# Kernel tuning notes

Hardware: AMD Instinct MI355X
Metric: run time of the kernel (lower is better)

Reference implementation:

```python
import jax, jax.numpy as jnp
import numpy as np

FILTER_WIDTH = 23
NSIG = 9.0
RATIO = 4.0
SUB_LOW_RATIO = 1.0
PCT = 3.0  # normalization_percentile_threshold


def _gaussian_kernel_2d(ksize, sigma):
    # matches cv2.getGaussianKernel for sigma > 0: normalized 1D gaussian, outer product
    i = np.arange(ksize, dtype=np.float64) - (ksize - 1) / 2.0
    k1 = np.exp(-(i ** 2) / (2.0 * sigma ** 2))
    k1 /= k1.sum()
    k2 = np.outer(k1, k1)
    return k2.astype(np.float32)


def setup_inputs() -> dict:
    key = jax.random.key(0)
    k1, k2 = jax.random.split(key)
    x = jax.random.normal(k1, (16, 3, 512, 512), dtype=jnp.float32)
    mask = jax.random.uniform(k2, (16, 1, 512, 512), dtype=jnp.float32)
    kernel = jnp.asarray(_gaussian_kernel_2d(FILTER_WIDTH, NSIG))[None, None]  # [1,1,23,23]
    return {"x": x, "mask": mask, "kernel": kernel}


def reference(x, mask, kernel):
    N, C, H, W = x.shape
    pad = FILTER_WIDTH // 2  # 11

    # --- median padding (torch.median = lower median -> sorted index (n-1)//2) ---
    flat = x.reshape(N, C, H * W)
    med = jnp.sort(flat, axis=-1)[:, :, (H * W - 1) // 2] + 0.2  # [N,C]
    med = med[:, :, None, None]
    xp = mask * x + (1.0 - mask) * med  # [N,C,H,W]

    # --- Gaussian low-pass: replication pad + depthwise conv (same kernel per channel) ---
    xpad = jnp.pad(xp, ((0, 0), (0, 0), (pad, pad), (pad, pad)), mode="edge")
    k = jnp.broadcast_to(kernel, (C, 1, FILTER_WIDTH, FILTER_WIDTH))
    gauss = jax.lax.conv_general_dilated(
        xpad, k, window_strides=(1, 1), padding="VALID", feature_group_count=C
    )  # [N,C,H,W]

    res = RATIO * (xp - SUB_LOW_RATIO * gauss)

    # --- per-(n,c) percentile normalization on 1/256-quantized copy ---
    temp = jnp.trunc(res * 256.0) / 256.0  # torch .int() truncates toward zero
    tflat = temp.reshape(N, C, H * W)
    lo = jnp.percentile(tflat, PCT, axis=-1)[:, :, None, None]
    hi = jnp.percentile(tflat, 100.0 - PCT, axis=-1)[:, :, None, None]
    res = (res - lo) / (hi - lo)

    # sub_mask=True
    return res * mask
```

## Files before the change

### kernel.cpp

```cpp
#include <hip/hip_runtime.h>

#define HW 262144
#define WID 512
#define PLANES 48
#define NCH 3
#define PAD 11
#define FW 23
#define XS 92

__device__ __forceinline__ float uniform_f(float v) {
  return __uint_as_float((unsigned)__builtin_amdgcn_readfirstlane((int)__float_as_uint(v)));
}

__global__ __launch_bounds__(256) void hist1_kernel(const float* __restrict__ x,
                                                    int* __restrict__ ghist1) {
  __shared__ int h[8192];
  const int p = blockIdx.x, s = blockIdx.y, tid = threadIdx.x;
  for (int i = tid; i < 8192; i += 256) h[i] = 0;
  __syncthreads();
  const float4* xv = (const float4*)(x + (size_t)p * HW + (size_t)s * (HW / 16));
#define H1(c) { int b = (int)(((c) + 8.0f) * 512.0f); b = min(max(b, 0), 8191); atomicAdd(&h[b], 1); }
  for (int i = tid; i < HW / 16 / 4; i += 256) {
    float4 v = xv[i];
    H1(v.x); H1(v.y); H1(v.z); H1(v.w);
  }
#undef H1
  __syncthreads();
  int* gh = ghist1 + p * 8192;
  const int st = (s * 512) & 8191;
  for (int k = tid; k < 8192; k += 256) {
    int i = (k + st) & 8191;
    int c = h[i];
    if (c) atomicAdd(&gh[i], c);
  }
}

__global__ __launch_bounds__(256) void scan_med_kernel(const int* __restrict__ ghist1,
                                                       float* __restrict__ med,
                                                       const float* __restrict__ kern,
                                                       float* __restrict__ k1g) {
  __shared__ int incl[256];
  __shared__ int s_chunk, s_base;
  const int p = blockIdx.x, t = threadIdx.x;
  if (p == 0 && t < FW) k1g[t] = kern[t * FW + PAD] / sqrtf(kern[PAD * FW + PAD]);
  const int* gh = ghist1 + p * 8192;
  int mysum = 0;
#pragma unroll
  for (int j = 0; j < 32; ++j) mysum += gh[t * 32 + j];
  incl[t] = mysum;
  __syncthreads();
  for (int off = 1; off < 256; off <<= 1) {
    int v = (t >= off) ? incl[t - off] : 0;
    __syncthreads();
    incl[t] += v;
    __syncthreads();
  }
  const int rank = 131072;
  {
    int excl = incl[t] - mysum;
    if (excl < rank && rank <= incl[t]) { s_chunk = t; s_base = rank - excl; }
  }
  __syncthreads();
  if (t < 64) {
    const int c = s_chunk, base = s_base;
    int cnt = (t < 32) ? gh[c * 32 + t] : 0;
    int pfx = cnt;
#pragma unroll
    for (int off = 1; off < 32; off <<= 1) {
      int u = __shfl_up(pfx, off, 64);
      if (t >= off) pfx += u;
    }
    unsigned long long m = __ballot(t < 32 && pfx >= base);
    int bin = c * 32 + (__ffsll((long long)m) - 1);
    if (t == 0) med[p] = -8.0f + ((float)bin + 0.5f) * 0.001953125f + 0.2f;
  }
}

__global__ __launch_bounds__(256) void conv_kernel(const float* __restrict__ x,
                                                   const float* __restrict__ mask,
                                                   const float* __restrict__ k1g,
                                                   const float* __restrict__ med,
                                                   float* __restrict__ res) {
  __shared__ float xs[86 * XS];
  const int z = blockIdx.z;
  const int n = z / NCH;
  const int tbx = blockIdx.x, tby = blockIdx.y;
  const int tid = threadIdx.x;

  float k1[FW];
#pragma unroll
  for (int t = 0; t < FW; ++t) k1[t] = uniform_f(k1g[t]);

  const float m_med = uniform_f(med[z]);
  const int gr0 = tby * 64 - PAD;
  const int gc0 = tbx * 64 - PAD;
  const float* xb = x + (size_t)z * HW;
  const float* mb = mask + (size_t)n * HW;
  for (int i = tid; i < 86 * 86; i += 256) {
    int r = i / 86, c = i - r * 86;
    int gr = min(max(gr0 + r, 0), WID - 1);
    int gc = min(max(gc0 + c, 0), WID - 1);
    int g = gr * WID + gc;
    float xv = xb[g], mv = mb[g];
    xs[r * XS + c] = fmaf(mv, xv - m_med, m_med);
  }
  __syncthreads();

  float ah[3][8];
#pragma unroll
  for (int it = 0; it < 3; ++it) {
    const int g = tid + (it << 8);
    if (g < 86 * 8) {
      const int r = g >> 3, c0 = (g & 7) << 3;
      const float* row = &xs[r * XS + c0];
      float w[32];
#pragma unroll
      for (int q = 0; q < 8; ++q) *(float4*)&w[q * 4] = *(const float4*)(row + q * 4);
#pragma unroll
      for (int j = 0; j < 8; ++j) ah[it][j] = 0.f;
#pragma unroll
      for (int t = 0; t < FW; ++t) {
        const float k = k1[t];
#pragma unroll
        for (int j = 0; j < 8; ++j) ah[it][j] = fmaf(k, w[t + j], ah[it][j]);
      }
    }
  }

  const int ct = (tid & 15) << 2;
  const int rt = (tid >> 4) << 2;
  float4 xpA[4], xpB[4];
#pragma unroll
  for (int j = 0; j < 4; ++j) {
    const float* xr = &xs[(rt + j + PAD) * XS + ct];
    xpA[j] = *(const float4*)(xr + 8);
    xpB[j] = *(const float4*)(xr + 12);
  }
  __syncthreads();

#pragma unroll
  for (int it = 0; it < 3; ++it) {
    const int g = tid + (it << 8);
    if (g < 86 * 8) {
      const int r = g >> 3, c0 = (g & 7) << 3;
      *(float4*)&xs[r * XS + c0] = make_float4(ah[it][0], ah[it][1], ah[it][2], ah[it][3]);
      *(float4*)&xs[r * XS + c0 + 4] = make_float4(ah[it][4], ah[it][5], ah[it][6], ah[it][7]);
    }
  }
  __syncthreads();

  float4 acc[4];
#pragma unroll
  for (int j = 0; j < 4; ++j) acc[j] = make_float4(0.f, 0.f, 0.f, 0.f);
#pragma unroll
  for (int tp = 0; tp < 26; ++tp) {
    float4 v = *(const float4*)&xs[(rt + tp) * XS + ct];
    const int jlo = (tp - 22 > 0) ? (tp - 22) : 0;
    const int jhi = (tp < 3) ? tp : 3;
#pragma unroll
    for (int j = jlo; j <= jhi; ++j) {
      float k = k1[tp - j];
      acc[j].x = fmaf(k, v.x, acc[j].x);
      acc[j].y = fmaf(k, v.y, acc[j].y);
      acc[j].z = fmaf(k, v.z, acc[j].z);
      acc[j].w = fmaf(k, v.w, acc[j].w);
    }
  }

  float* rb = res + (size_t)z * HW + (size_t)(tby * 64 + rt) * WID + tbx * 64 + ct;
#pragma unroll
  for (int j = 0; j < 4; ++j) {
    float4 o;
    o.x = 4.0f * (xpA[j].w - acc[j].x);
    o.y = 4.0f * (xpB[j].x - acc[j].y);
    o.z = 4.0f * (xpB[j].y - acc[j].z);
    o.w = 4.0f * (xpB[j].z - acc[j].w);
    *(float4*)(rb + (size_t)j * WID) = o;
  }
}

__global__ __launch_bounds__(256) void hist_kernel(const float* __restrict__ res,
                                                   int* __restrict__ ghist) {
  __shared__ int h[8192];
  const int p = blockIdx.x, s = blockIdx.y, tid = threadIdx.x;
  for (int i = tid; i < 8192; i += 256) h[i] = 0;
  __syncthreads();
  const float4* rv = (const float4*)(res + (size_t)p * HW + (size_t)s * (HW / 16));
#define HADD(c) { int b = (int)((c) * 256.0f) + 4096; b = min(max(b, 0), 8191); atomicAdd(&h[b], 1); }
  for (int i = tid; i < HW / 16 / 4; i += 256) {
    float4 v = rv[i];
    HADD(v.x); HADD(v.y); HADD(v.z); HADD(v.w);
  }
#undef HADD
  __syncthreads();
  int* gh = ghist + p * 8192;
  const int st = (s * 512) & 8191;
  for (int k = tid; k < 8192; k += 256) {
    int i = (k + st) & 8191;
    int c = h[i];
    if (c) atomicAdd(&gh[i], c);
  }
}

__global__ __launch_bounds__(256) void pct_kernel(const int* __restrict__ ghist,
                                                  float* __restrict__ lo_out,
                                                  float* __restrict__ inv_out) {
  __shared__ int incl[256];
  __shared__ int s_chunk, s_base;
  __shared__ float s_v[4];
  const int p = blockIdx.x, t = threadIdx.x;
  const int* gh = ghist + p * 8192;
  int mysum = 0;
#pragma unroll
  for (int j = 0; j < 32; ++j) mysum += gh[t * 32 + j];
  incl[t] = mysum;
  __syncthreads();
  for (int off = 1; off < 256; off <<= 1) {
    int v = (t >= off) ? incl[t - off] : 0;
    __syncthreads();
    incl[t] += v;
    __syncthreads();
  }
  const int ranks[4] = {7865, 7866, 254279, 254280};
#pragma unroll
  for (int r = 0; r < 4; ++r) {
    const int rank = ranks[r];
    int excl = incl[t] - mysum;
    if (excl < rank && rank <= incl[t]) { s_chunk = t; s_base = rank - excl; }
    __syncthreads();
    if (t < 64) {
      const int c = s_chunk, base = s_base;
      int cnt = (t < 32) ? gh[c * 32 + t] : 0;
      int pfx = cnt;
#pragma unroll
      for (int off = 1; off < 32; off <<= 1) {
        int u = __shfl_up(pfx, off, 64);
        if (t >= off) pfx += u;
      }
      unsigned long long m = __ballot(t < 32 && pfx >= base);
      int bin = c * 32 + (__ffsll((long long)m) - 1);
      if (t == 0) s_v[r] = (float)(bin - 4096) * 0.00390625f;
    }
    __syncthreads();
  }
  if (t == 0) {
    const double fl = 0.29, fh = 0.71;
    double lov = (double)s_v[0] + fl * ((double)s_v[1] - (double)s_v[0]);
    double hiv = (double)s_v[2] + fh * ((double)s_v[3] - (double)s_v[2]);
    lo_out[p] = (float)lov;
    inv_out[p] = (float)(1.0 / (hiv - lov));
  }
}

__global__ __launch_bounds__(256) void final_kernel(float* __restrict__ res,
                                                    const float* __restrict__ mask,
                                                    const float* __restrict__ lo,
                                                    const float* __restrict__ inv) {
  const int i = blockIdx.x * 256 + threadIdx.x;
  const int e = i << 2;
  const int z = e >> 18;
  const int n = z / NCH;
  const int hw = e & (HW - 1);
  float4 r = ((const float4*)res)[i];
  float4 m = *(const float4*)(mask + (size_t)n * HW + hw);
  const float l = lo[z];
  const float iv = inv[z];
  float4 o;
  o.x = (r.x - l) * iv * m.x;
  o.y = (r.y - l) * iv * m.y;
  o.z = (r.z - l) * iv * m.z;
  o.w = (r.w - l) * iv * m.w;
  ((float4*)res)[i] = o;
}

extern "C" void kernel_launch(void* const* d_in, const int* in_sizes, int n_in,
                              void* d_out, int out_size, void* d_ws, size_t ws_size,
                              hipStream_t stream) {
  (void)in_sizes; (void)n_in; (void)out_size; (void)ws_size;
  const float* x = (const float*)d_in[0];
  const float* mask = (const float*)d_in[1];
  const float* kern = (const float*)d_in[2];
  float* out = (float*)d_out;

  int* hist = (int*)d_ws;
  int* ghist1 = hist + PLANES * 8192;
  float* med = (float*)(ghist1 + PLANES * 8192);
  float* lo = med + PLANES;
  float* inv = lo + PLANES;
  float* k1g = inv + PLANES;

  hipMemsetAsync(hist, 0, (size_t)PLANES * (8192 + 8192) * sizeof(int), stream);
  hist1_kernel<<<dim3(PLANES, 16), 256, 0, stream>>>(x, ghist1);
  scan_med_kernel<<<PLANES, 256, 0, stream>>>(ghist1, med, kern, k1g);
  conv_kernel<<<dim3(8, 8, PLANES), 256, 0, stream>>>(x, mask, k1g, med, out);
  hist_kernel<<<dim3(PLANES, 16), 256, 0, stream>>>(out, hist);
  pct_kernel<<<PLANES, 256, 0, stream>>>(hist, lo, inv);
  final_kernel<<<(HW * PLANES / 4 + 255) / 256, 256, 0, stream>>>(out, mask, lo, inv);
}
```

Measured before the change: 209.6 us.

## Fuse scan kernels into histogram kernels via last-block tickets and halve conv tile height

```diff
diff --git a/kernel.cpp b/kernel.cpp
--- a/kernel.cpp
+++ b/kernel.cpp
@@ -7,15 +7,26 @@
 #define PAD 11
 #define FW 23
 #define XS 92
+#define TROWS 54
 
 __device__ __forceinline__ float uniform_f(float v) {
   return __uint_as_float((unsigned)__builtin_amdgcn_readfirstlane((int)__float_as_uint(v)));
 }
+__device__ __forceinline__ int aload(const int* p) {
+  return __hip_atomic_load(p, __ATOMIC_RELAXED, __HIP_MEMORY_SCOPE_AGENT);
+}
 
 __global__ __launch_bounds__(256) void hist1_kernel(const float* __restrict__ x,
-                                                    int* __restrict__ ghist1) {
+                                                    int* __restrict__ ghist1,
+                                                    float* __restrict__ med,
+                                                    const float* __restrict__ kern,
+                                                    float* __restrict__ k1g,
+                                                    int* __restrict__ tick) {
   __shared__ int h[8192];
+  __shared__ int s_chunk, s_base, s_last;
   const int p = blockIdx.x, s = blockIdx.y, tid = threadIdx.x;
+  if (p == 0 && s == 0 && tid < FW)
+    k1g[tid] = kern[tid * FW + PAD] / sqrtf(kern[PAD * FW + PAD]);
   for (int i = tid; i < 8192; i += 256) h[i] = 0;
   __syncthreads();
   const float4* xv = (const float4*)(x + (size_t)p * HW + (size_t)s * (HW / 16));
@@ -33,55 +44,49 @@
     int c = h[i];
     if (c) atomicAdd(&gh[i], c);
   }
-}
-
-__global__ __launch_bounds__(256) void scan_med_kernel(const int* __restrict__ ghist1,
-                                                       float* __restrict__ med,
-                                                       const float* __restrict__ kern,
-                                                       float* __restrict__ k1g) {
-  __shared__ int incl[256];
-  __shared__ int s_chunk, s_base;
-  const int p = blockIdx.x, t = threadIdx.x;
-  if (p == 0 && t < FW) k1g[t] = kern[t * FW + PAD] / sqrtf(kern[PAD * FW + PAD]);
-  const int* gh = ghist1 + p * 8192;
+  __threadfence();
+  if (tid == 0) s_last = atomicAdd(&tick[p], 1);
+  __syncthreads();
+  if (s_last != 15) return;
+
   int mysum = 0;
 #pragma unroll
-  for (int j = 0; j < 32; ++j) mysum += gh[t * 32 + j];
-  incl[t] = mysum;
+  for (int j = 0; j < 32; ++j) mysum += aload(&gh[tid * 32 + j]);
+  h[tid] = mysum;
   __syncthreads();
   for (int off = 1; off < 256; off <<= 1) {
-    int v = (t >= off) ? incl[t - off] : 0;
-    __syncthreads();
-    incl[t] += v;
+    int v = (tid >= off) ? h[tid - off] : 0;
+    __syncthreads();
+    h[tid] += v;
     __syncthreads();
   }
   const int rank = 131072;
   {
-    int excl = incl[t] - mysum;
-    if (excl < rank && rank <= incl[t]) { s_chunk = t; s_base = rank - excl; }
-  }
-  __syncthreads();
-  if (t < 64) {
+    int excl = h[tid] - mysum;
+    if (excl < rank && rank <= h[tid]) { s_chunk = tid; s_base = rank - excl; }
+  }
+  __syncthreads();
+  if (tid < 64) {
     const int c = s_chunk, base = s_base;
-    int cnt = (t < 32) ? gh[c * 32 + t] : 0;
+    int cnt = (tid < 32) ? aload(&gh[c * 32 + tid]) : 0;
     int pfx = cnt;
 #pragma unroll
     for (int off = 1; off < 32; off <<= 1) {
       int u = __shfl_up(pfx, off, 64);
-      if (t >= off) pfx += u;
-    }
-    unsigned long long m = __ballot(t < 32 && pfx >= base);
+      if (tid >= off) pfx += u;
+    }
+    unsigned long long m = __ballot(tid < 32 && pfx >= base);
     int bin = c * 32 + (__ffsll((long long)m) - 1);
-    if (t == 0) med[p] = -8.0f + ((float)bin + 0.5f) * 0.001953125f + 0.2f;
-  }
-}
-
-__global__ __launch_bounds__(256) void conv_kernel(const float* __restrict__ x,
-                                                   const float* __restrict__ mask,
-                                                   const float* __restrict__ k1g,
-                                                   const float* __restrict__ med,
-                                                   float* __restrict__ res) {
-  __shared__ float xs[86 * XS];
+    if (tid == 0) med[p] = -8.0f + ((float)bin + 0.5f) * 0.001953125f + 0.2f;
+  }
+}
+
+__global__ __launch_bounds__(256, 8) void conv_kernel(const float* __restrict__ x,
+                                                      const float* __restrict__ mask,
+                                                      const float* __restrict__ k1g,
+                                                      const float* __restrict__ med,
+                                                      float* __restrict__ res) {
+  __shared__ float xs[TROWS * XS];
   const int z = blockIdx.z;
   const int n = z / NCH;
   const int tbx = blockIdx.x, tby = blockIdx.y;
@@ -92,11 +97,11 @@
   for (int t = 0; t < FW; ++t) k1[t] = uniform_f(k1g[t]);
 
   const float m_med = uniform_f(med[z]);
-  const int gr0 = tby * 64 - PAD;
+  const int gr0 = tby * 32 - PAD;
   const int gc0 = tbx * 64 - PAD;
   const float* xb = x + (size_t)z * HW;
   const float* mb = mask + (size_t)n * HW;
-  for (int i = tid; i < 86 * 86; i += 256) {
+  for (int i = tid; i < TROWS * 86; i += 256) {
     int r = i / 86, c = i - r * 86;
     int gr = min(max(gr0 + r, 0), WID - 1);
     int gc = min(max(gc0 + c, 0), WID - 1);
@@ -106,11 +111,11 @@
   }
   __syncthreads();
 
-  float ah[3][8];
-#pragma unroll
-  for (int it = 0; it < 3; ++it) {
+  float ah[2][8];
+#pragma unroll
+  for (int it = 0; it < 2; ++it) {
     const int g = tid + (it << 8);
-    if (g < 86 * 8) {
+    if (g < TROWS * 8) {
       const int r = g >> 3, c0 = (g & 7) << 3;
       const float* row = &xs[r * XS + c0];
       float w[32];
@@ -128,10 +133,10 @@
   }
 
   const int ct = (tid & 15) << 2;
-  const int rt = (tid >> 4) << 2;
-  float4 xpA[4], xpB[4];
-#pragma unroll
-  for (int j = 0; j < 4; ++j) {
+  const int rt = (tid >> 4) << 1;
+  float4 xpA[2], xpB[2];
+#pragma unroll
+  for (int j = 0; j < 2; ++j) {
     const float* xr = &xs[(rt + j + PAD) * XS + ct];
     xpA[j] = *(const float4*)(xr + 8);
     xpB[j] = *(const float4*)(xr + 12);
@@ -139,9 +144,9 @@
   __syncthreads();
 
 #pragma unroll
-  for (int it = 0; it < 3; ++it) {
+  for (int it = 0; it < 2; ++it) {
     const int g = tid + (it << 8);
-    if (g < 86 * 8) {
+    if (g < TROWS * 8) {
       const int r = g >> 3, c0 = (g & 7) << 3;
       *(float4*)&xs[r * XS + c0] = make_float4(ah[it][0], ah[it][1], ah[it][2], ah[it][3]);
       *(float4*)&xs[r * XS + c0 + 4] = make_float4(ah[it][4], ah[it][5], ah[it][6], ah[it][7]);
@@ -149,14 +154,14 @@
   }
   __syncthreads();
 
-  float4 acc[4];
-#pragma unroll
-  for (int j = 0; j < 4; ++j) acc[j] = make_float4(0.f, 0.f, 0.f, 0.f);
-#pragma unroll
-  for (int tp = 0; tp < 26; ++tp) {
+  float4 acc[2];
+#pragma unroll
+  for (int j = 0; j < 2; ++j) acc[j] = make_float4(0.f, 0.f, 0.f, 0.f);
+#pragma unroll
+  for (int tp = 0; tp < 24; ++tp) {
     float4 v = *(const float4*)&xs[(rt + tp) * XS + ct];
     const int jlo = (tp - 22 > 0) ? (tp - 22) : 0;
-    const int jhi = (tp < 3) ? tp : 3;
+    const int jhi = (tp < 1) ? tp : 1;
 #pragma unroll
     for (int j = jlo; j <= jhi; ++j) {
       float k = k1[tp - j];
@@ -167,9 +172,9 @@
     }
   }
 
-  float* rb = res + (size_t)z * HW + (size_t)(tby * 64 + rt) * WID + tbx * 64 + ct;
-#pragma unroll
-  for (int j = 0; j < 4; ++j) {
+  float* rb = res + (size_t)z * HW + (size_t)(tby * 32 + rt) * WID + tbx * 64 + ct;
+#pragma unroll
+  for (int j = 0; j < 2; ++j) {
     float4 o;
     o.x = 4.0f * (xpA[j].w - acc[j].x);
     o.y = 4.0f * (xpB[j].x - acc[j].y);
@@ -180,8 +185,13 @@
 }
 
 __global__ __launch_bounds__(256) void hist_kernel(const float* __restrict__ res,
-                                                   int* __restrict__ ghist) {
+                                                   int* __restrict__ ghist,
+                                                   float* __restrict__ lo_out,
+                                                   float* __restrict__ inv_out,
+                                                   int* __restrict__ tick) {
   __shared__ int h[8192];
+  __shared__ int s_chunk, s_base, s_last;
+  __shared__ float s_v[4];
   const int p = blockIdx.x, s = blockIdx.y, tid = threadIdx.x;
   for (int i = tid; i < 8192; i += 256) h[i] = 0;
   __syncthreads();
@@ -200,50 +210,45 @@
     int c = h[i];
     if (c) atomicAdd(&gh[i], c);
   }
-}
-
-__global__ __launch_bounds__(256) void pct_kernel(const int* __restrict__ ghist,
-                                                  float* __restrict__ lo_out,
-                                                  float* __restrict__ inv_out) {
-  __shared__ int incl[256];
-  __shared__ int s_chunk, s_base;
-  __shared__ float s_v[4];
-  const int p = blockIdx.x, t = threadIdx.x;
-  const int* gh = ghist + p * 8192;
+  __threadfence();
+  if (tid == 0) s_last = atomicAdd(&tick[p], 1);
+  __syncthreads();
+  if (s_last != 15) return;
+
   int mysum = 0;
 #pragma unroll
-  for (int j = 0; j < 32; ++j) mysum += gh[t * 32 + j];
-  incl[t] = mysum;
+  for (int j = 0; j < 32; ++j) mysum += aload(&gh[tid * 32 + j]);
+  h[tid] = mysum;
   __syncthreads();
   for (int off = 1; off < 256; off <<= 1) {
-    int v = (t >= off) ? incl[t - off] : 0;
-    __syncthreads();
-    incl[t] += v;
+    int v = (tid >= off) ? h[tid - off] : 0;
+    __syncthreads();
+    h[tid] += v;
     __syncthreads();
   }
   const int ranks[4] = {7865, 7866, 254279, 254280};
 #pragma unroll
   for (int r = 0; r < 4; ++r) {
     const int rank = ranks[r];
-    int excl = incl[t] - mysum;
-    if (excl < rank && rank <= incl[t]) { s_chunk = t; s_base = rank - excl; }
-    __syncthreads();
-    if (t < 64) {
+    int excl = h[tid] - mysum;
+    if (excl < rank && rank <= h[tid]) { s_chunk = tid; s_base = rank - excl; }
+    __syncthreads();
+    if (tid < 64) {
       const int c = s_chunk, base = s_base;
-      int cnt = (t < 32) ? gh[c * 32 + t] : 0;
+      int cnt = (tid < 32) ? aload(&gh[c * 32 + tid]) : 0;
       int pfx = cnt;
 #pragma unroll
       for (int off = 1; off < 32; off <<= 1) {
         int u = __shfl_up(pfx, off, 64);
-        if (t >= off) pfx += u;
+        if (tid >= off) pfx += u;
       }
-      unsigned long long m = __ballot(t < 32 && pfx >= base);
+      unsigned long long m = __ballot(tid < 32 && pfx >= base);
       int bin = c * 32 + (__ffsll((long long)m) - 1);
-      if (t == 0) s_v[r] = (float)(bin - 4096) * 0.00390625f;
-    }
-    __syncthreads();
-  }
-  if (t == 0) {
+      if (tid == 0) s_v[r] = (float)(bin - 4096) * 0.00390625f;
+    }
+    __syncthreads();
+  }
+  if (tid == 0) {
     const double fl = 0.29, fh = 0.71;
     double lov = (double)s_v[0] + fl * ((double)s_v[1] - (double)s_v[0]);
     double hiv = (double)s_v[2] + fh * ((double)s_v[3] - (double)s_v[2]);
@@ -284,16 +289,16 @@
 
   int* hist = (int*)d_ws;
   int* ghist1 = hist + PLANES * 8192;
-  float* med = (float*)(ghist1 + PLANES * 8192);
+  int* tick1 = ghist1 + PLANES * 8192;
+  int* tick2 = tick1 + PLANES;
+  float* med = (float*)(tick2 + PLANES);
   float* lo = med + PLANES;
   float* inv = lo + PLANES;
   float* k1g = inv + PLANES;
 
-  hipMemsetAsync(hist, 0, (size_t)PLANES * (8192 + 8192) * sizeof(int), stream);
-  hist1_kernel<<<dim3(PLANES, 16), 256, 0, stream>>>(x, ghist1);
-  scan_med_kernel<<<PLANES, 256, 0, stream>>>(ghist1, med, kern, k1g);
-  conv_kernel<<<dim3(8, 8, PLANES), 256, 0, stream>>>(x, mask, k1g, med, out);
-  hist_kernel<<<dim3(PLANES, 16), 256, 0, stream>>>(out, hist);
-  pct_kernel<<<PLANES, 256, 0, stream>>>(hist, lo, inv);
+  hipMemsetAsync(hist, 0, ((size_t)PLANES * (8192 + 8192) + 2 * PLANES) * sizeof(int), stream);
+  hist1_kernel<<<dim3(PLANES, 16), 256, 0, stream>>>(x, ghist1, med, kern, k1g, tick1);
+  conv_kernel<<<dim3(8, 16, PLANES), 256, 0, stream>>>(x, mask, k1g, med, out);
+  hist_kernel<<<dim3(PLANES, 16), 256, 0, stream>>>(out, hist, lo, inv, tick2);
   final_kernel<<<(HW * PLANES / 4 + 255) / 256, 256, 0, stream>>>(out, mask, lo, inv);
 }
```

After: 304.8 us. 1.45x slower.

## Replace global histogram atomics with packed 16-bit partial histograms reduced in scan

Applied to the files above, without the earlier changes.

```diff
diff --git a/kernel.cpp b/kernel.cpp
--- a/kernel.cpp
+++ b/kernel.cpp
@@ -7,46 +7,69 @@
 #define PAD 11
 #define FW 23
 #define XS 92
+#define NSUB 16
 
 __device__ __forceinline__ float uniform_f(float v) {
   return __uint_as_float((unsigned)__builtin_amdgcn_readfirstlane((int)__float_as_uint(v)));
 }
 
 __global__ __launch_bounds__(256) void hist1_kernel(const float* __restrict__ x,
-                                                    int* __restrict__ ghist1) {
+                                                    ushort* __restrict__ part) {
   __shared__ int h[8192];
   const int p = blockIdx.x, s = blockIdx.y, tid = threadIdx.x;
   for (int i = tid; i < 8192; i += 256) h[i] = 0;
   __syncthreads();
-  const float4* xv = (const float4*)(x + (size_t)p * HW + (size_t)s * (HW / 16));
+  const float4* xv = (const float4*)(x + (size_t)p * HW + (size_t)s * (HW / NSUB));
 #define H1(c) { int b = (int)(((c) + 8.0f) * 512.0f); b = min(max(b, 0), 8191); atomicAdd(&h[b], 1); }
-  for (int i = tid; i < HW / 16 / 4; i += 256) {
+  for (int i = tid; i < HW / NSUB / 4; i += 256) {
     float4 v = xv[i];
     H1(v.x); H1(v.y); H1(v.z); H1(v.w);
   }
 #undef H1
   __syncthreads();
-  int* gh = ghist1 + p * 8192;
-  const int st = (s * 512) & 8191;
-  for (int k = tid; k < 8192; k += 256) {
-    int i = (k + st) & 8191;
-    int c = h[i];
-    if (c) atomicAdd(&gh[i], c);
-  }
-}
-
-__global__ __launch_bounds__(256) void scan_med_kernel(const int* __restrict__ ghist1,
+  uint4* out = (uint4*)(part + ((size_t)p * NSUB + s) * 8192);
+  for (int k = tid; k < 1024; k += 256) {
+    int4 a = *(const int4*)&h[k * 8];
+    int4 b = *(const int4*)&h[k * 8 + 4];
+    uint4 w;
+    w.x = (unsigned)a.x | ((unsigned)a.y << 16);
+    w.y = (unsigned)a.z | ((unsigned)a.w << 16);
+    w.z = (unsigned)b.x | ((unsigned)b.y << 16);
+    w.w = (unsigned)b.z | ((unsigned)b.w << 16);
+    out[k] = w;
+  }
+}
+
+__global__ __launch_bounds__(256) void scan_med_kernel(const ushort* __restrict__ part,
                                                        float* __restrict__ med,
                                                        const float* __restrict__ kern,
                                                        float* __restrict__ k1g) {
+  __shared__ int hsum[8192];
   __shared__ int incl[256];
   __shared__ int s_chunk, s_base;
   const int p = blockIdx.x, t = threadIdx.x;
   if (p == 0 && t < FW) k1g[t] = kern[t * FW + PAD] / sqrtf(kern[PAD * FW + PAD]);
-  const int* gh = ghist1 + p * 8192;
+  const uint4* pr = (const uint4*)(part + (size_t)p * NSUB * 8192);
+  for (int idx = t; idx < 1024; idx += 256) {
+    int a0=0,a1=0,a2=0,a3=0,a4=0,a5=0,a6=0,a7=0;
+#pragma unroll
+    for (int s = 0; s < NSUB; ++s) {
+      uint4 v = pr[(size_t)s * 1024 + idx];
+      a0 += (int)(v.x & 0xffff); a1 += (int)(v.x >> 16);
+      a2 += (int)(v.y & 0xffff); a3 += (int)(v.y >> 16);
+      a4 += (int)(v.z & 0xffff); a5 += (int)(v.z >> 16);
+      a6 += (int)(v.w & 0xffff); a7 += (int)(v.w >> 16);
+    }
+    int* hb = &hsum[idx * 8];
+    hb[0]=a0; hb[1]=a1; hb[2]=a2; hb[3]=a3; hb[4]=a4; hb[5]=a5; hb[6]=a6; hb[7]=a7;
+  }
+  __syncthreads();
   int mysum = 0;
 #pragma unroll
-  for (int j = 0; j < 32; ++j) mysum += gh[t * 32 + j];
+  for (int j = 0; j < 32; j += 4) {
+    int4 v = *(const int4*)&hsum[t * 32 + j];
+    mysum += v.x + v.y + v.z + v.w;
+  }
   incl[t] = mysum;
   __syncthreads();
   for (int off = 1; off < 256; off <<= 1) {
@@ -63,7 +86,7 @@
   __syncthreads();
   if (t < 64) {
     const int c = s_chunk, base = s_base;
-    int cnt = (t < 32) ? gh[c * 32 + t] : 0;
+    int cnt = (t < 32) ? hsum[c * 32 + t] : 0;
     int pfx = cnt;
 #pragma unroll
     for (int off = 1; off < 32; off <<= 1) {
@@ -180,39 +203,61 @@
 }
 
 __global__ __launch_bounds__(256) void hist_kernel(const float* __restrict__ res,
-                                                   int* __restrict__ ghist) {
+                                                   ushort* __restrict__ part) {
   __shared__ int h[8192];
   const int p = blockIdx.x, s = blockIdx.y, tid = threadIdx.x;
   for (int i = tid; i < 8192; i += 256) h[i] = 0;
   __syncthreads();
-  const float4* rv = (const float4*)(res + (size_t)p * HW + (size_t)s * (HW / 16));
+  const float4* rv = (const float4*)(res + (size_t)p * HW + (size_t)s * (HW / NSUB));
 #define HADD(c) { int b = (int)((c) * 256.0f) + 4096; b = min(max(b, 0), 8191); atomicAdd(&h[b], 1); }
-  for (int i = tid; i < HW / 16 / 4; i += 256) {
+  for (int i = tid; i < HW / NSUB / 4; i += 256) {
     float4 v = rv[i];
     HADD(v.x); HADD(v.y); HADD(v.z); HADD(v.w);
   }
 #undef HADD
   __syncthreads();
-  int* gh = ghist + p * 8192;
-  const int st = (s * 512) & 8191;
-  for (int k = tid; k < 8192; k += 256) {
-    int i = (k + st) & 8191;
-    int c = h[i];
-    if (c) atomicAdd(&gh[i], c);
-  }
-}
-
-__global__ __launch_bounds__(256) void pct_kernel(const int* __restrict__ ghist,
+  uint4* out = (uint4*)(part + ((size_t)p * NSUB + s) * 8192);
+  for (int k = tid; k < 1024; k += 256) {
+    int4 a = *(const int4*)&h[k * 8];
+    int4 b = *(const int4*)&h[k * 8 + 4];
+    uint4 w;
+    w.x = (unsigned)a.x | ((unsigned)a.y << 16);
+    w.y = (unsigned)a.z | ((unsigned)a.w << 16);
+    w.z = (unsigned)b.x | ((unsigned)b.y << 16);
+    w.w = (unsigned)b.z | ((unsigned)b.w << 16);
+    out[k] = w;
+  }
+}
+
+__global__ __launch_bounds__(256) void pct_kernel(const ushort* __restrict__ part,
                                                   float* __restrict__ lo_out,
                                                   float* __restrict__ inv_out) {
+  __shared__ int hsum[8192];
   __shared__ int incl[256];
   __shared__ int s_chunk, s_base;
   __shared__ float s_v[4];
   const int p = blockIdx.x, t = threadIdx.x;
-  const int* gh = ghist + p * 8192;
+  const uint4* pr = (const uint4*)(part + (size_t)p * NSUB * 8192);
+  for (int idx = t; idx < 1024; idx += 256) {
+    int a0=0,a1=0,a2=0,a3=0,a4=0,a5=0,a6=0,a7=0;
+#pragma unroll
+    for (int s = 0; s < NSUB; ++s) {
+      uint4 v = pr[(size_t)s * 1024 + idx];
+      a0 += (int)(v.x & 0xffff); a1 += (int)(v.x >> 16);
+      a2 += (int)(v.y & 0xffff); a3 += (int)(v.y >> 16);
+      a4 += (int)(v.z & 0xffff); a5 += (int)(v.z >> 16);
+      a6 += (int)(v.w & 0xffff); a7 += (int)(v.w >> 16);
+    }
+    int* hb = &hsum[idx * 8];
+    hb[0]=a0; hb[1]=a1; hb[2]=a2; hb[3]=a3; hb[4]=a4; hb[5]=a5; hb[6]=a6; hb[7]=a7;
+  }
+  __syncthreads();
   int mysum = 0;
 #pragma unroll
-  for (int j = 0; j < 32; ++j) mysum += gh[t * 32 + j];
+  for (int j = 0; j < 32; j += 4) {
+    int4 v = *(const int4*)&hsum[t * 32 + j];
+    mysum += v.x + v.y + v.z + v.w;
+  }
   incl[t] = mysum;
   __syncthreads();
   for (int off = 1; off < 256; off <<= 1) {
@@ -230,7 +275,7 @@
     __syncthreads();
     if (t < 64) {
       const int c = s_chunk, base = s_base;
-      int cnt = (t < 32) ? gh[c * 32 + t] : 0;
+      int cnt = (t < 32) ? hsum[c * 32 + t] : 0;
       int pfx = cnt;
 #pragma unroll
       for (int off = 1; off < 32; off <<= 1) {
@@ -282,18 +327,16 @@
   const float* kern = (const float*)d_in[2];
   float* out = (float*)d_out;
 
-  int* hist = (int*)d_ws;
-  int* ghist1 = hist + PLANES * 8192;
-  float* med = (float*)(ghist1 + PLANES * 8192);
+  ushort* part = (ushort*)d_ws;
+  float* med = (float*)(part + (size_t)PLANES * NSUB * 8192);
   float* lo = med + PLANES;
   float* inv = lo + PLANES;
   float* k1g = inv + PLANES;
 
-  hipMemsetAsync(hist, 0, (size_t)PLANES * (8192 + 8192) * sizeof(int), stream);
-  hist1_kernel<<<dim3(PLANES, 16), 256, 0, stream>>>(x, ghist1);
-  scan_med_kernel<<<PLANES, 256, 0, stream>>>(ghist1, med, kern, k1g);
+  hist1_kernel<<<dim3(PLANES, NSUB), 256, 0, stream>>>(x, part);
+  scan_med_kernel<<<PLANES, 256, 0, stream>>>(part, med, kern, k1g);
   conv_kernel<<<dim3(8, 8, PLANES), 256, 0, stream>>>(x, mask, k1g, med, out);
-  hist_kernel<<<dim3(PLANES, 16), 256, 0, stream>>>(out, hist);
-  pct_kernel<<<PLANES, 256, 0, stream>>>(hist, lo, inv);
+  hist_kernel<<<dim3(PLANES, NSUB), 256, 0, stream>>>(out, part);
+  pct_kernel<<<PLANES, 256, 0, stream>>>(part, lo, inv);
   final_kernel<<<(HW * PLANES / 4 + 255) / 256, 256, 0, stream>>>(out, mask, lo, inv);
 }
```

Result: faster. 201.0 us (-4.1%).
